# Kernel optimization log

Measured on AMD Instinct MI355X. Metric: run time of the kernel, lower is better.

## Reference

```python
import jax, jax.numpy as jnp
import numpy as np

MC = 16384
N_STEPS = 120
PERIOD = 30
N_MAT = 4
N_STR = 21
WIDTH_DIFF = 50
WIDTH_VAN = 30
WIDTH_EXO = 20
N_HIDDEN = 3  # n_layers=4 -> input layer + 3 hidden layers + output layer
R = 0.05
TIMEGRID = jnp.asarray(np.linspace(0.0, 1.0, N_STEPS + 1).astype(np.float32))
STRIKES = jnp.asarray(np.linspace(0.8, 1.2, N_STR).astype(np.float32))


def _init_net(key, d_in, width, d_out):
    ks = jax.random.split(key, 6)
    f = lambda k, shape, fan: jax.random.normal(k, shape, jnp.float32) / np.sqrt(fan).astype(np.float32)
    return dict(
        W0=f(ks[0], (N_MAT, d_in, width), d_in),
        b0=f(ks[1], (N_MAT, width), width),
        hW=f(ks[2], (N_MAT, N_HIDDEN, width, width), width),
        hb=f(ks[3], (N_MAT, N_HIDDEN, width), width),
        Wo=f(ks[4], (N_MAT, width, d_out), width),
        bo=f(ks[5], (N_MAT, d_out), width),
    )


def setup_inputs() -> dict:
    key = jax.random.key(0)
    kz, kd, kv, ke = jax.random.split(key, 4)
    inp = {
        "S0": jnp.ones((1,), jnp.float32),
        "z": jax.random.normal(kz, (MC, N_STEPS), jnp.float32),
    }
    for name, net in (("d", _init_net(kd, 2, WIDTH_DIFF, 1)),
                      ("v", _init_net(kv, 2, WIDTH_VAN, N_STR * N_MAT)),
                      ("e", _init_net(ke, N_STEPS + 2, WIDTH_EXO, 1))):
        for pn, arr in net.items():
            inp[name + pn] = arr
    inp["MC_samples"] = MC
    inp["ind_T"] = N_STEPS
    inp["period_length"] = PERIOD
    return inp


def _mlp(x, W0, b0, hW, hb, Wo, bo, softplus_out):
    h = jax.nn.relu(x @ W0 + b0)
    for k in range(hW.shape[0]):  # static small number of hidden layers
        h = jax.nn.relu(h @ hW[k] + hb[k])
    y = h @ Wo + bo
    return jax.nn.softplus(y) if softplus_out else y


def _forward(S0, z, dW0, db0, dhW, dhb, dWo, dbo,
             vW0, vb0, vhW, vhb, vWo, vbo,
             eW0, eb0, ehW, ehb, eWo, ebo,
             MC_samples, ind_T, period_length, remat=False):
    sg = jax.lax.stop_gradient
    S_init = jnp.ones((MC_samples, 1), jnp.float32) * S0
    path0 = jnp.zeros((MC_samples, N_STEPS + 1), jnp.float32).at[:, 0].set(S_init[:, 0])
    zeros_mat = jnp.zeros((N_MAT, N_STR), jnp.float32)

    def step(carry, i):
        S_old, cv_v, cv_e, run_max, path, pv, pvv = carry
        idx = (i - 1) // period_length
        t0 = TIMEGRID[i - 1]
        h = TIMEGRID[i] - TIMEGRID[i - 1]
        sqh = jnp.sqrt(h)
        dWn = sqh * jax.lax.dynamic_slice_in_dim(z, i - 1, 1, 1)  # (MC,1)
        t = jnp.full_like(S_old, t0)
        diff = _mlp(jnp.concatenate([t, S_old], 1),
                    dW0[idx], db0[idx], dhW[idx], dhb[idx], dWo[idx], dbo[idx], True)
        Sd, diffd = sg(S_old), sg(diff)
        S_new = (S_old
                 + R * S_old * h / (1.0 + R * Sd * sqh)
                 + S_old * diff * dWn / (1.0 + Sd * diffd * sqh))
        disc = jnp.exp(-R * t0)
        cv_v = cv_v + disc * Sd * diffd * dWn * _mlp(
            jnp.concatenate([t, Sd], 1),
            vW0[idx], vb0[idx], vhW[idx], vhb[idx], vWo[idx], vbo[idx], False)
        cv_e = cv_e + disc * Sd * diffd * dWn * _mlp(
            jnp.concatenate([t, path], 1),
            eW0[idx], eb0[idx], ehW[idx], ehb[idx], eWo[idx], ebo[idx], False)
        path = jax.lax.dynamic_update_slice(path, sg(S_new), (0, i))
        run_max = jnp.maximum(run_max, S_new)
        # vanilla prices at maturities (i multiple of period_length)
        ind_m = i // period_length - 1
        disc_i = jnp.exp(-R * TIMEGRID[i])
        cv_row = jax.lax.dynamic_slice_in_dim(
            cv_v.reshape(MC_samples, N_MAT, N_STR), ind_m, 1, 1)[:, 0, :]
        pr = disc_i * jnp.maximum(S_new - STRIKES[None, :], 0.0) - cv_row  # (MC, N_STR)
        is_mat = (i % period_length) == 0
        pv = jnp.where(is_mat, jax.lax.dynamic_update_index_in_dim(pv, pr.mean(0), ind_m, 0), pv)
        pvv = jnp.where(is_mat, jax.lax.dynamic_update_index_in_dim(pvv, jnp.var(pr, axis=0, ddof=1), ind_m, 0), pvv)
        return (S_new, cv_v, cv_e, run_max, path, pv, pvv), None

    body = jax.checkpoint(step) if remat else step
    carry0 = (S_init,
              jnp.zeros((MC_samples, N_STR * N_MAT), jnp.float32),
              jnp.zeros((MC_samples, 1), jnp.float32),
              S_init, path0, zeros_mat, zeros_mat)
    (S_T, cv_v, cv_e, run_max, path, pv, pvv), _ = jax.lax.scan(
        body, carry0, jnp.arange(1, ind_T + 1))

    sgv = jax.lax.stop_gradient
    exotic = run_max - S_T
    discT = jnp.exp(-R * TIMEGRID[ind_T])
    e = discT * exotic
    error = sgv(e) - jnp.mean(sgv(e)) - sgv(cv_e)
    price_exo = e - cv_e
    return pv, pvv, price_exo, price_exo.mean(), jnp.var(price_exo, ddof=1), error


def reference(S0, z, dW0, db0, dhW, dhb, dWo, dbo,
              vW0, vb0, vhW, vhb, vWo, vbo,
              eW0, eb0, ehW, ehb, eWo, ebo,
              MC_samples, ind_T, period_length):
    return _forward(S0, z, dW0, db0, dhW, dhb, dWo, dbo,
                    vW0, vb0, vhW, vhb, vWo, vbo,
                    eW0, eb0, ehW, ehb, eWo, ebo,
                    MC_samples, ind_T, period_length)
```

## Files before the change

kernel.cpp:

```cpp
#include <hip/hip_runtime.h>
#include <math.h>

#define MC      16384
#define NSTEPS  120
#define PER     30
#define NMAT    4
#define NSTR    21
#define RRATE   0.05f
#define NBLK    512
#define NSAMP   32

typedef short short8  __attribute__((ext_vector_type(8)));
typedef short short4v __attribute__((ext_vector_type(4)));
typedef float f32x4   __attribute__((ext_vector_type(4)));

#define WS_PRPART 0
#define WS_EPART  (NMAT*NSTR*2*NBLK)
#define WS_MEANE  (WS_EPART + NBLK)

#define OUT_PV    0
#define OUT_PVV   84
#define OUT_PEXO  168
#define OUT_MEAN  16552
#define OUT_VAR   16553
#define OUT_ERR   16554

__device__ __forceinline__ float tgridf(int i)  { return (float)((double)i * (1.0/120.0)); }
__device__ __forceinline__ float strikef(int s) { return (float)(0.8 + (double)s * 0.02); }
__device__ __forceinline__ float softplusf(float x){
  return fmaxf(x, 0.0f) + log1pf(expf(-fabsf(x)));
}
__device__ __forceinline__ unsigned short f2bf(float f){
  unsigned u = __builtin_bit_cast(unsigned, f);
  unsigned r = (u + 0x7FFFu + ((u>>16)&1u)) >> 16;
  return (unsigned short)r;
}
__device__ __forceinline__ float bf2f(unsigned short u){
  return __builtin_bit_cast(float, ((unsigned)u)<<16);
}
__device__ __forceinline__ int swaddr(int row, int slot, int inner){
  return row*256 + (((slot + row) & 15) << 4) + inner;
}
__device__ __forceinline__ short8 rdA(const unsigned short* H, int mt, int base, int lane){
  int addr = swaddr(mt*16 + (lane&15), base + (lane>>4), 0);
  return *(const short8*)((const char*)H + addr);
}
__device__ __forceinline__ f32x4 mm(short8 a, short8 b, f32x4 c){
  return __builtin_amdgcn_mfma_f32_16x16x32_bf16(a, b, c, 0, 0, 0);
}
__device__ __forceinline__ void stD(unsigned short* H, int colbase, int mt, int lane,
                                    f32x4 acc, float bias, bool relu){
  int col  = colbase + (lane & 15);
  int slot = col >> 3, inner = (col & 7)*2;
  #pragma unroll
  for (int i2=0;i2<4;++i2){
    int rw = mt*16 + ((lane>>4)<<2) + i2;
    float v = acc[i2] + bias;
    if (relu) v = fmaxf(v, 0.0f);
    *(unsigned short*)((char*)H + swaddr(rw, slot, inner)) = f2bf(v);
  }
}
__device__ __forceinline__ short8 mkB(const float* __restrict__ W, int ldn, int KV, int NV,
                                      int kt, int n0, int lane){
  short8 r;
  #pragma unroll
  for (int i2=0;i2<8;++i2){
    int k = kt*32 + ((lane>>4)<<3) + i2;
    int n = n0 + (lane & 15);
    float w = (k<KV && n<NV) ? W[k*ldn + n] : 0.0f;
    r[i2] = (short)f2bf(w);
  }
  return r;
}

extern "C" __global__ void __launch_bounds__(256,2) mc_main(
    const float* __restrict__ S0p, const float* __restrict__ z,
    const float* __restrict__ dW0, const float* __restrict__ db0,
    const float* __restrict__ dhW, const float* __restrict__ dhb,
    const float* __restrict__ dWo, const float* __restrict__ dbo,
    const float* __restrict__ vW0, const float* __restrict__ vb0,
    const float* __restrict__ vhW, const float* __restrict__ vhb,
    const float* __restrict__ vWo, const float* __restrict__ vbo,
    const float* __restrict__ eW0, const float* __restrict__ eb0,
    const float* __restrict__ ehW, const float* __restrict__ ehb,
    const float* __restrict__ eWo, const float* __restrict__ ebo,
    float* __restrict__ out, float* __restrict__ ws)
{
  __shared__ unsigned short Hb0[NSAMP*128];
  __shared__ unsigned short Hb1[NSAMP*128];
  __shared__ float vh3f[NSAMP*40];
  __shared__ float zper[NSAMP*30];
  __shared__ float eW0per[NMAT*600];
  __shared__ float dW0s[NMAT*128];
  __shared__ float db0s[NMAT*64];
  __shared__ float vW0s[NMAT*64];
  __shared__ float vb0s[NMAT*32];
  __shared__ float eW0ts[NMAT*20];
  __shared__ float eb0s[NMAT*20];
  __shared__ float dWoL[64];
  __shared__ float eWoL[32];
  __shared__ float Sb[NSAMP], Cb[NSAMP], ebuf[NSAMP];
  __shared__ float part[2*84*2];

  const int tid  = threadIdx.x;
  const int lane = tid & 63;
  const int wid  = __builtin_amdgcn_readfirstlane(tid >> 6);
  const int blk  = blockIdx.x;
  const int r    = tid >> 3;
  const int cc   = tid & 7;

  for (int q=tid; q<NMAT*128; q+=256){ int mat=q>>7, rw=(q>>6)&1, j=q&63; dW0s[q] = (j<50)? dW0[mat*100+rw*50+j] : 0.f; }
  for (int q=tid; q<NMAT*64;  q+=256){ int mat=q>>6, j=q&63;              db0s[q] = (j<50)? db0[mat*50+j] : 0.f; }
  for (int q=tid; q<NMAT*64;  q+=256){ int mat=q>>6, rw=(q>>5)&1, j=q&31; vW0s[q] = (j<30)? vW0[mat*60+rw*30+j] : 0.f; }
  for (int q=tid; q<NMAT*32;  q+=256){ int mat=q>>5, j=q&31;              vb0s[q] = (j<30)? vb0[mat*30+j] : 0.f; }
  if (tid < NMAT*20){ int mat=tid/20, j=tid%20; eW0ts[tid]=eW0[mat*2440+j]; eb0s[tid]=eb0[mat*20+j]; }

  const int  ntd = wid;
  const bool isv = (wid < 2);
  const int  ntq = wid & 1;

  const float S0v = S0p[0];
  float S = S0v, runmax = S0v, cvE = 0.f, C = 0.f;
  f32x4 rr[3];
  #pragma unroll
  for (int q=0;q<3;++q){ rr[q][0]=0.f; rr[q][1]=0.f; rr[q][2]=0.f; rr[q][3]=0.f; }
  float aE[NMAT][4];
  #pragma unroll
  for (int mt2=0;mt2<NMAT;++mt2){ aE[mt2][0]=0.f; aE[mt2][1]=0.f; aE[mt2][2]=0.f; aE[mt2][3]=0.f; }
  float G_[4] = {0.f,0.f,0.f,0.f};

  #pragma unroll 1
  for (int p=0;p<NMAT;++p){
    for (int q=tid; q<NSAMP*30; q+=256){ int r2=q/30, c2=q%30; zper[q] = z[(size_t)(blk*NSAMP+r2)*NSTEPS + p*30 + c2]; }
    for (int q=tid; q<NMAT*600; q+=256){ int mat=q/600, k=q%600; eW0per[q] = eW0[mat*2440 + p*600 + 20 + k]; }
    if (tid < 64)              dWoL[tid] = (tid<50)? dWo[p*50+tid] : 0.f;
    else if (tid < 96){ int j=tid-64; eWoL[j] = (j<20)? eWo[p*20+j] : 0.f; }

    const float dboS = dbo[p], eboS = ebo[p];

    const float* dhWp = dhW + p*7500;
    short8 Bd00 = mkB(dhWp,      50,50,50, 0, ntd*16, lane);
    short8 Bd01 = mkB(dhWp,      50,50,50, 1, ntd*16, lane);
    short8 Bd10 = mkB(dhWp+2500, 50,50,50, 0, ntd*16, lane);
    short8 Bd11 = mkB(dhWp+2500, 50,50,50, 1, ntd*16, lane);
    short8 Bd20 = mkB(dhWp+5000, 50,50,50, 0, ntd*16, lane);
    short8 Bd21 = mkB(dhWp+5000, 50,50,50, 1, ntd*16, lane);
    const int nd = ntd*16 + (lane&15);
    float biasD0 = (nd<50)? dhb[p*150 +      nd] : 0.f;
    float biasD1 = (nd<50)? dhb[p*150 + 50 + nd] : 0.f;
    float biasD2 = (nd<50)? dhb[p*150 +100 + nd] : 0.f;
    const float* qW    = isv ? (vhW + p*2700) : (ehW + p*1200);
    const int    qstep = isv ? 900 : 400;
    const int    qN    = isv ? 30  : 20;
    short8 Bq0 = mkB(qW,         qN,qN,qN, 0, ntq*16, lane);
    short8 Bq1 = mkB(qW+qstep,   qN,qN,qN, 0, ntq*16, lane);
    short8 Bq2 = mkB(qW+2*qstep, qN,qN,qN, 0, ntq*16, lane);
    const float* qb = isv ? (vhb + p*90) : (ehb + p*60);
    const int nq = ntq*16 + (lane&15);
    float biasQ0 = (nq<qN)? qb[       nq] : 0.f;
    float biasQ1 = (nq<qN)? qb[qN   + nq] : 0.f;
    float biasQ2 = (nq<qN)? qb[2*qN + nq] : 0.f;

    const int qbase = isv ? 8 : 12;
    const int qcolb = (isv?64:96) + ntq*16;

    __syncthreads();

    #pragma unroll 1
    for (int ii=1; ii<=PER; ++ii){
      const float t0  = tgridf(p*PER + ii - 1);
      const float t1  = tgridf(p*PER + ii);
      const float h   = t1 - t0;
      const float sqh = sqrtf(h);

      {
        short8 hv;
        #pragma unroll
        for (int k=0;k<8;++k){
          int j = cc*8 + k;
          float u = fmaxf(fmaf(t0, dW0s[p*128+j], fmaf(S, dW0s[p*128+64+j], db0s[p*64+j])), 0.f);
          hv[k] = (short)f2bf(u);
        }
        *(short8*)((char*)Hb0 + swaddr(r, cc, 0)) = hv;
        short4v vv;
        #pragma unroll
        for (int k=0;k<4;++k){
          int j = cc*4 + k;
          float u = fmaxf(fmaf(t0, vW0s[p*64+j], fmaf(S, vW0s[p*64+32+j], vb0s[p*32+j])), 0.f);
          vv[k] = (short)f2bf(u);
        }
        *(short4v*)((char*)Hb0 + swaddr(r, 8+(cc>>1), (cc&1)*8)) = vv;
        short4v ev = {0,0,0,0};
        if (cc < 5){
          const int o = (ii-1)*20 + cc*4;
          f32x4 w0 = *(const f32x4*)&eW0per[        o];
          f32x4 w1 = *(const f32x4*)&eW0per[ 600 +  o];
          f32x4 w2 = *(const f32x4*)&eW0per[1200 +  o];
          f32x4 w3 = *(const f32x4*)&eW0per[1800 +  o];
          #pragma unroll
          for (int k=0;k<4;++k){
            aE[0][k] = fmaf(S, w0[k], aE[0][k]);
            aE[1][k] = fmaf(S, w1[k], aE[1][k]);
            aE[2][k] = fmaf(S, w2[k], aE[2][k]);
            aE[3][k] = fmaf(S, w3[k], aE[3][k]);
            float a = (p==0)?aE[0][k]:(p==1)?aE[1][k]:(p==2)?aE[2][k]:aE[3][k];
            int j = cc*4 + k;
            float e0 = fmaxf(t0*eW0ts[p*20+j] + a + eb0s[p*20+j], 0.f);
            ev[k] = (short)f2bf(e0);
          }
        }
        *(short4v*)((char*)Hb0 + swaddr(r, 12+(cc>>1), (cc&1)*8)) = ev;
      }
      __syncthreads();
      {
        short8 a00=rdA(Hb0,0,0,lane), a01=rdA(Hb0,0,4,lane);
        short8 a10=rdA(Hb0,1,0,lane), a11=rdA(Hb0,1,4,lane);
        f32x4 c0={0.f,0.f,0.f,0.f}, c1={0.f,0.f,0.f,0.f};
        c0=mm(a00,Bd00,c0); c0=mm(a01,Bd01,c0);
        c1=mm(a10,Bd00,c1); c1=mm(a11,Bd01,c1);
        stD(Hb1, ntd*16, 0, lane, c0, biasD0, true);
        stD(Hb1, ntd*16, 1, lane, c1, biasD0, true);
        short8 q0=rdA(Hb0,0,qbase,lane), q1=rdA(Hb0,1,qbase,lane);
        f32x4 cq0={0.f,0.f,0.f,0.f}, cq1={0.f,0.f,0.f,0.f};
        cq0=mm(q0,Bq0,cq0); cq1=mm(q1,Bq0,cq1);
        stD(Hb1, qcolb, 0, lane, cq0, biasQ0, true);
        stD(Hb1, qcolb, 1, lane, cq1, biasQ0, true);
      }
      __syncthreads();
      {
        short8 a00=rdA(Hb1,0,0,lane), a01=rdA(Hb1,0,4,lane);
        short8 a10=rdA(Hb1,1,0,lane), a11=rdA(Hb1,1,4,lane);
        f32x4 c0={0.f,0.f,0.f,0.f}, c1={0.f,0.f,0.f,0.f};
        c0=mm(a00,Bd10,c0); c0=mm(a01,Bd11,c0);
        c1=mm(a10,Bd10,c1); c1=mm(a11,Bd11,c1);
        stD(Hb0, ntd*16, 0, lane, c0, biasD1, true);
        stD(Hb0, ntd*16, 1, lane, c1, biasD1, true);
        short8 q0=rdA(Hb1,0,qbase,lane), q1=rdA(Hb1,1,qbase,lane);
        f32x4 cq0={0.f,0.f,0.f,0.f}, cq1={0.f,0.f,0.f,0.f};
        cq0=mm(q0,Bq1,cq0); cq1=mm(q1,Bq1,cq1);
        stD(Hb0, qcolb, 0, lane, cq0, biasQ1, true);
        stD(Hb0, qcolb, 1, lane, cq1, biasQ1, true);
      }
      __syncthreads();
      {
        short8 a00=rdA(Hb0,0,0,lane), a01=rdA(Hb0,0,4,lane);
        short8 a10=rdA(Hb0,1,0,lane), a11=rdA(Hb0,1,4,lane);
        f32x4 c0={0.f,0.f,0.f,0.f}, c1={0.f,0.f,0.f,0.f};
        c0=mm(a00,Bd20,c0); c0=mm(a01,Bd21,c0);
        c1=mm(a10,Bd20,c1); c1=mm(a11,Bd21,c1);
        stD(Hb1, ntd*16, 0, lane, c0, biasD2, true);
        stD(Hb1, ntd*16, 1, lane, c1, biasD2, true);
        short8 q0=rdA(Hb0,0,qbase,lane), q1=rdA(Hb0,1,qbase,lane);
        f32x4 cq0={0.f,0.f,0.f,0.f}, cq1={0.f,0.f,0.f,0.f};
        cq0=mm(q0,Bq2,cq0); cq1=mm(q1,Bq2,cq1);
        if (isv){
          #pragma unroll
          for (int i2=0;i2<4;++i2){
            int r0 = ((lane>>4)<<2) + i2;
            vh3f[ r0      *40 + ntq*16 + (lane&15)] = fmaxf(cq0[i2] + biasQ2, 0.f);
            vh3f[(16+r0)  *40 + ntq*16 + (lane&15)] = fmaxf(cq1[i2] + biasQ2, 0.f);
          }
        } else {
          stD(Hb1, qcolb, 0, lane, cq0, biasQ2, true);
          stD(Hb1, qcolb, 1, lane, cq1, biasQ2, true);
        }
      }
      __syncthreads();
      {
        float yp = 0.f;
        {
          short8 hv = *(const short8*)((const char*)Hb1 + swaddr(r, cc, 0));
          #pragma unroll
          for (int k=0;k<8;++k) yp = fmaf(bf2f((unsigned short)hv[k]), dWoL[cc*8+k], yp);
        }
        float yep = 0.f;
        if (cc < 5){
          short4v hv = *(const short4v*)((const char*)Hb1 + swaddr(r, 12+(cc>>1), (cc&1)*8));
          #pragma unroll
          for (int k=0;k<4;++k) yep = fmaf(bf2f((unsigned short)hv[k]), eWoL[cc*4+k], yep);
        }
        #pragma unroll
        for (int mk=1; mk<8; mk<<=1){ yp += __shfl_xor(yp, mk); yep += __shfl_xor(yep, mk); }
        const float y    = yp + dboS;
        const float diff = softplusf(y);
        const float zv   = zper[r*30 + (ii-1)];
        const float dWn  = sqh * zv;
        const float d1 = 1.f + RRATE*S*sqh;
        const float d2 = 1.f + S*diff*sqh;
        const float Snew = S + RRATE*S*h/d1 + S*diff*dWn/d2;
        const float disc = expf(-RRATE*t0);
        const float coef = disc * S * diff * dWn;
        cvE = fmaf(coef, yep + eboS, cvE);
        C += coef;
        runmax = fmaxf(runmax, Snew);
        {
          f32x4 vv = *(const f32x4*)&vh3f[r*40 + cc*4];
          #pragma unroll
          for (int k=0;k<4;++k) G_[k] = fmaf(coef, vv[k], G_[k]);
        }
        S = Snew;

        if (ii==PER){
          short4v gv;
          #pragma unroll
          for (int k=0;k<4;++k){ gv[k] = (short)f2bf(G_[k]); G_[k] = 0.f; }
          *(short4v*)((char*)Hb0 + swaddr(r, cc>>1, (cc&1)*8)) = gv;
          if (cc==0){ Sb[r] = S; Cb[r] = C; }
          C = 0.f;
        }
      }

      if (ii==PER){
        __syncthreads();
        const float disc_i = expf(-RRATE*t1);
        const float* vWop = vWo + p*2520;
        const float* vbop = vbo + p*84;
        #pragma unroll
        for (int q3=0;q3<3;++q3){
          const int T = wid*3 + q3;
          const int mtr = T/6, ntr = T%6;
          short8 a = rdA(Hb0, mtr, 0, lane);
          const int col = ntr*16 + (lane&15);
          short8 bw;
          #pragma unroll
          for (int i2=0;i2<8;++i2){
            int k = ((lane>>4)<<3)+i2;
            float w = (k<30 && col<84) ? vWop[k*84+col] : 0.f;
            bw[i2] = (short)f2bf(w);
          }
          f32x4 d4 = {0.f,0.f,0.f,0.f};
          d4 = mm(a,bw,d4);
          const float vb = (col<84)? vbop[col] : 0.f;
          const int s = col - p*NSTR;
          const bool inr = (s>=0) && (s<NSTR) && (col<84);
          const float K = strikef(s);
          float ssum=0.f, ssq=0.f;
          #pragma unroll
          for (int i2=0;i2<4;++i2){
            int row = mtr*16 + ((lane>>4)<<2) + i2;
            rr[q3][i2] += d4[i2] + Cb[row]*vb;
            if (inr){
              float pr = disc_i*fmaxf(Sb[row]-K,0.f) - rr[q3][i2];
              ssum += pr; ssq = fmaf(pr,pr,ssq);
            }
          }
          ssum += __shfl_down(ssum,16); ssum += __shfl_down(ssum,32);
          ssq  += __shfl_down(ssq ,16); ssq  += __shfl_down(ssq ,32);
          if (inr && lane<16){
            part[(mtr*84+col)*2+0] = ssum;
            part[(mtr*84+col)*2+1] = ssq;
          }
        }
        __syncthreads();
        if (tid < NSTR){
          int cidx = p*NSTR + tid;
          ws[WS_PRPART + (cidx*2+0)*NBLK + blk] = part[cidx*2] + part[(84+cidx)*2];
        } else if (tid >= 64 && tid < 64+NSTR){
          int cidx = p*NSTR + (tid-64);
          ws[WS_PRPART + (cidx*2+1)*NBLK + blk] = part[cidx*2+1] + part[(84+cidx)*2+1];
        }
      }
    }
  }

  if (cc==0){
    const float discT = expf(-RRATE);
    const float e = discT * (runmax - S);
    out[OUT_PEXO + blk*NSAMP + r] = e - cvE;
    ebuf[r] = e;
  }
  __syncthreads();
  if (tid < 32){
    float se = ebuf[tid];
    se += __shfl_down(se,16); se += __shfl_down(se,8);
    se += __shfl_down(se,4);  se += __shfl_down(se,2); se += __shfl_down(se,1);
    if (tid==0) ws[WS_EPART + blk] = se;
  }
}

extern "C" __global__ void fin_pv(const float* __restrict__ ws, float* __restrict__ out){
  const int t = threadIdx.x;
  if (t >= NMAT*NSTR) return;
  float sum=0.0f, ssq=0.0f;
  for (int b=0;b<NBLK;++b){
    sum += ws[WS_PRPART + (t*2+0)*NBLK + b];
    ssq += ws[WS_PRPART + (t*2+1)*NBLK + b];
  }
  out[OUT_PV  + t] = sum * (1.0f/MC);
  out[OUT_PVV + t] = (ssq - sum*sum*(1.0f/MC)) * (1.0f/(MC-1));
}

extern "C" __global__ void fin_pe(float* out, float* ws){
  __shared__ float sA[4], sB[4], sC[4];
  const int t = threadIdx.x;
  float sum=0.0f, ssq=0.0f;
  for (int idx=t; idx<MC; idx+=256){
    const float v = out[OUT_PEXO+idx];
    sum += v; ssq = fmaf(v,v,ssq);
  }
  float es = ws[WS_EPART + t] + ws[WS_EPART + 256 + t];
  for (int o=32;o>0;o>>=1){
    sum += __shfl_down(sum,o);
    ssq += __shfl_down(ssq,o);
    es  += __shfl_down(es,o);
  }
  const int w=t>>6, lane=t&63;
  if (lane==0){ sA[w]=sum; sB[w]=ssq; sC[w]=es; }
  __syncthreads();
  if (t==0){
    const float s=sA[0]+sA[1]+sA[2]+sA[3];
    const float q=sB[0]+sB[1]+sB[2]+sB[3];
    const float e=sC[0]+sC[1]+sC[2]+sC[3];
    out[OUT_MEAN]=s*(1.0f/MC);
    out[OUT_VAR]=(q - s*s*(1.0f/MC))*(1.0f/(MC-1));
    ws[WS_MEANE]=e*(1.0f/MC);
  }
}

extern "C" __global__ void fin_err(float* out, const float* __restrict__ ws){
  const int m = blockIdx.x*blockDim.x + threadIdx.x;
  if (m < MC) out[OUT_ERR+m] = out[OUT_PEXO+m] - ws[WS_MEANE];
}

extern "C" void kernel_launch(void* const* d_in, const int* in_sizes, int n_in,
                              void* d_out, int out_size, void* d_ws, size_t ws_size,
                              hipStream_t stream){
  (void)in_sizes; (void)n_in; (void)out_size; (void)ws_size;
  const float* S0 =(const float*)d_in[0];
  const float* z  =(const float*)d_in[1];
  const float* dW0=(const float*)d_in[2];
  const float* db0=(const float*)d_in[3];
  const float* dhW=(const float*)d_in[4];
  const float* dhb=(const float*)d_in[5];
  const float* dWo=(const float*)d_in[6];
  const float* dbo=(const float*)d_in[7];
  const float* vW0=(const float*)d_in[8];
  const float* vb0=(const float*)d_in[9];
  const float* vhW=(const float*)d_in[10];
  const float* vhb=(const float*)d_in[11];
  const float* vWo=(const float*)d_in[12];
  const float* vbo=(const float*)d_in[13];
  const float* eW0=(const float*)d_in[14];
  const float* eb0=(const float*)d_in[15];
  const float* ehW=(const float*)d_in[16];
  const float* ehb=(const float*)d_in[17];
  const float* eWo=(const float*)d_in[18];
  const float* ebo=(const float*)d_in[19];
  float* out=(float*)d_out;
  float* ws =(float*)d_ws;

  mc_main<<<dim3(NBLK),dim3(256),0,stream>>>(S0,z,dW0,db0,dhW,dhb,dWo,dbo,
                                             vW0,vb0,vhW,vhb,vWo,vbo,
                                             eW0,eb0,ehW,ehb,eWo,ebo,out,ws);
  fin_pv <<<dim3(1), dim3(128),0,stream>>>(ws,out);
  fin_pe <<<dim3(1), dim3(256),0,stream>>>(out,ws);
  fin_err<<<dim3(64),dim3(256),0,stream>>>(out,ws);
}
```

Before: 489.4 us.

## Fold MLP biases into MFMA via constant-one column and spill B-fragments to LDS

Adds a constant 1 feature column to each hidden activation tile and places each layer's bias in the matching weight row, so the MFMA computes the bias. This removes per-element bias adds and the separate C accumulator and Cb buffer for the van output. Some B fragments (third diffusion layer and the Q-net weights) now live in LDS instead of registers, which lowers VGPR pressure but adds LDS reads in every step. The approach depends on bf16 rounding of the bias, which changes numerics slightly, and on spare padded columns being free.

```diff
diff --git a/kernel.cpp b/kernel.cpp
--- a/kernel.cpp
+++ b/kernel.cpp
@@ -49,25 +49,43 @@
   return __builtin_amdgcn_mfma_f32_16x16x32_bf16(a, b, c, 0, 0, 0);
 }
 __device__ __forceinline__ void stD(unsigned short* H, int colbase, int mt, int lane,
-                                    f32x4 acc, float bias, bool relu){
+                                    f32x4 acc, bool relu){
   int col  = colbase + (lane & 15);
   int slot = col >> 3, inner = (col & 7)*2;
   #pragma unroll
   for (int i2=0;i2<4;++i2){
     int rw = mt*16 + ((lane>>4)<<2) + i2;
-    float v = acc[i2] + bias;
+    float v = acc[i2];
     if (relu) v = fmaxf(v, 0.0f);
     *(unsigned short*)((char*)H + swaddr(rw, slot, inner)) = f2bf(v);
   }
 }
-__device__ __forceinline__ short8 mkB(const float* __restrict__ W, int ldn, int KV, int NV,
-                                      int kt, int n0, int lane){
+__device__ __forceinline__ short8 mkBd(const float* __restrict__ W, const float* __restrict__ bias,
+                                       int n0, int kt, int lane){
   short8 r;
+  int n = n0 + (lane&15);
   #pragma unroll
   for (int i2=0;i2<8;++i2){
     int k = kt*32 + ((lane>>4)<<3) + i2;
-    int n = n0 + (lane & 15);
-    float w = (k<KV && n<NV) ? W[k*ldn + n] : 0.0f;
+    float w;
+    if (k<50)       w = (n<50)? W[k*50+n] : 0.f;
+    else if (k==50) w = (n<50)? bias[n] : ((n==50)? 1.f : 0.f);
+    else            w = 0.f;
+    r[i2] = (short)f2bf(w);
+  }
+  return r;
+}
+__device__ __forceinline__ short8 mkBq(const float* __restrict__ W, const float* __restrict__ bias,
+                                       int KV, int n0, int lane){
+  short8 r;
+  int n = n0 + (lane&15);
+  #pragma unroll
+  for (int i2=0;i2<8;++i2){
+    int k = ((lane>>4)<<3) + i2;
+    float w;
+    if (k<KV)       w = (n<KV)? W[k*KV+n] : 0.f;
+    else if (k==KV) w = (n<KV)? bias[n] : ((n==KV)? 1.f : 0.f);
+    else            w = 0.f;
     r[i2] = (short)f2bf(w);
   }
   return r;
@@ -88,6 +106,8 @@
 {
   __shared__ unsigned short Hb0[NSAMP*128];
   __shared__ unsigned short Hb1[NSAMP*128];
+  __shared__ short8 BqL[4][3][64];
+  __shared__ short8 BdL[4][2][64];
   __shared__ float vh3f[NSAMP*40];
   __shared__ float zper[NSAMP*30];
   __shared__ float eW0per[NMAT*600];
@@ -99,7 +119,7 @@
   __shared__ float eb0s[NMAT*20];
   __shared__ float dWoL[64];
   __shared__ float eWoL[32];
-  __shared__ float Sb[NSAMP], Cb[NSAMP], ebuf[NSAMP];
+  __shared__ float Sb[NSAMP], ebuf[NSAMP];
   __shared__ float part[2*84*2];
 
   const int tid  = threadIdx.x;
@@ -110,9 +130,9 @@
   const int cc   = tid & 7;
 
   for (int q=tid; q<NMAT*128; q+=256){ int mat=q>>7, rw=(q>>6)&1, j=q&63; dW0s[q] = (j<50)? dW0[mat*100+rw*50+j] : 0.f; }
-  for (int q=tid; q<NMAT*64;  q+=256){ int mat=q>>6, j=q&63;              db0s[q] = (j<50)? db0[mat*50+j] : 0.f; }
+  for (int q=tid; q<NMAT*64;  q+=256){ int mat=q>>6, j=q&63;              db0s[q] = (j<50)? db0[mat*50+j] : ((j==50)? 1.f : 0.f); }
   for (int q=tid; q<NMAT*64;  q+=256){ int mat=q>>6, rw=(q>>5)&1, j=q&31; vW0s[q] = (j<30)? vW0[mat*60+rw*30+j] : 0.f; }
-  for (int q=tid; q<NMAT*32;  q+=256){ int mat=q>>5, j=q&31;              vb0s[q] = (j<30)? vb0[mat*30+j] : 0.f; }
+  for (int q=tid; q<NMAT*32;  q+=256){ int mat=q>>5, j=q&31;              vb0s[q] = (j<30)? vb0[mat*30+j] : ((j==30)? 1.f : 0.f); }
   if (tid < NMAT*20){ int mat=tid/20, j=tid%20; eW0ts[tid]=eW0[mat*2440+j]; eb0s[tid]=eb0[mat*20+j]; }
 
   const int  ntd = wid;
@@ -120,7 +140,7 @@
   const int  ntq = wid & 1;
 
   const float S0v = S0p[0];
-  float S = S0v, runmax = S0v, cvE = 0.f, C = 0.f;
+  float S = S0v, runmax = S0v, cvE = 0.f;
   f32x4 rr[3];
   #pragma unroll
   for (int q=0;q<3;++q){ rr[q][0]=0.f; rr[q][1]=0.f; rr[q][2]=0.f; rr[q][3]=0.f; }
@@ -139,28 +159,22 @@
     const float dboS = dbo[p], eboS = ebo[p];
 
     const float* dhWp = dhW + p*7500;
-    short8 Bd00 = mkB(dhWp,      50,50,50, 0, ntd*16, lane);
-    short8 Bd01 = mkB(dhWp,      50,50,50, 1, ntd*16, lane);
-    short8 Bd10 = mkB(dhWp+2500, 50,50,50, 0, ntd*16, lane);
-    short8 Bd11 = mkB(dhWp+2500, 50,50,50, 1, ntd*16, lane);
-    short8 Bd20 = mkB(dhWp+5000, 50,50,50, 0, ntd*16, lane);
-    short8 Bd21 = mkB(dhWp+5000, 50,50,50, 1, ntd*16, lane);
-    const int nd = ntd*16 + (lane&15);
-    float biasD0 = (nd<50)? dhb[p*150 +      nd] : 0.f;
-    float biasD1 = (nd<50)? dhb[p*150 + 50 + nd] : 0.f;
-    float biasD2 = (nd<50)? dhb[p*150 +100 + nd] : 0.f;
-    const float* qW    = isv ? (vhW + p*2700) : (ehW + p*1200);
-    const int    qstep = isv ? 900 : 400;
-    const int    qN    = isv ? 30  : 20;
-    short8 Bq0 = mkB(qW,         qN,qN,qN, 0, ntq*16, lane);
-    short8 Bq1 = mkB(qW+qstep,   qN,qN,qN, 0, ntq*16, lane);
-    short8 Bq2 = mkB(qW+2*qstep, qN,qN,qN, 0, ntq*16, lane);
-    const float* qb = isv ? (vhb + p*90) : (ehb + p*60);
-    const int nq = ntq*16 + (lane&15);
-    float biasQ0 = (nq<qN)? qb[       nq] : 0.f;
-    float biasQ1 = (nq<qN)? qb[qN   + nq] : 0.f;
-    float biasQ2 = (nq<qN)? qb[2*qN + nq] : 0.f;
-
+    const float* dhbp = dhb + p*150;
+    short8 Bd00 = mkBd(dhWp,      dhbp,     ntd*16, 0, lane);
+    short8 Bd01 = mkBd(dhWp,      dhbp,     ntd*16, 1, lane);
+    short8 Bd10 = mkBd(dhWp+2500, dhbp+50,  ntd*16, 0, lane);
+    short8 Bd11 = mkBd(dhWp+2500, dhbp+50,  ntd*16, 1, lane);
+    BdL[wid][0][lane] = mkBd(dhWp+5000, dhbp+100, ntd*16, 0, lane);
+    BdL[wid][1][lane] = mkBd(dhWp+5000, dhbp+100, ntd*16, 1, lane);
+    {
+      const float* qW    = isv ? (vhW + p*2700) : (ehW + p*1200);
+      const float* qb    = isv ? (vhb + p*90)   : (ehb + p*60);
+      const int    qstep = isv ? 900 : 400;
+      const int    qN    = isv ? 30  : 20;
+      BqL[wid][0][lane] = mkBq(qW,         qb,        qN, ntq*16, lane);
+      BqL[wid][1][lane] = mkBq(qW+qstep,   qb+qN,     qN, ntq*16, lane);
+      BqL[wid][2][lane] = mkBq(qW+2*qstep, qb+2*qN,   qN, ntq*16, lane);
+    }
     const int qbase = isv ? 8 : 12;
     const int qcolb = (isv?64:96) + ntq*16;
 
@@ -208,6 +222,8 @@
             float e0 = fmaxf(t0*eW0ts[p*20+j] + a + eb0s[p*20+j], 0.f);
             ev[k] = (short)f2bf(e0);
           }
+        } else if (cc == 5){
+          ev[0] = (short)0x3F80;
         }
         *(short4v*)((char*)Hb0 + swaddr(r, 12+(cc>>1), (cc&1)*8)) = ev;
       }
@@ -218,13 +234,14 @@
         f32x4 c0={0.f,0.f,0.f,0.f}, c1={0.f,0.f,0.f,0.f};
         c0=mm(a00,Bd00,c0); c0=mm(a01,Bd01,c0);
         c1=mm(a10,Bd00,c1); c1=mm(a11,Bd01,c1);
-        stD(Hb1, ntd*16, 0, lane, c0, biasD0, true);
-        stD(Hb1, ntd*16, 1, lane, c1, biasD0, true);
+        stD(Hb1, ntd*16, 0, lane, c0, true);
+        stD(Hb1, ntd*16, 1, lane, c1, true);
+        short8 Bq = BqL[wid][0][lane];
         short8 q0=rdA(Hb0,0,qbase,lane), q1=rdA(Hb0,1,qbase,lane);
         f32x4 cq0={0.f,0.f,0.f,0.f}, cq1={0.f,0.f,0.f,0.f};
-        cq0=mm(q0,Bq0,cq0); cq1=mm(q1,Bq0,cq1);
-        stD(Hb1, qcolb, 0, lane, cq0, biasQ0, true);
-        stD(Hb1, qcolb, 1, lane, cq1, biasQ0, true);
+        cq0=mm(q0,Bq,cq0); cq1=mm(q1,Bq,cq1);
+        stD(Hb1, qcolb, 0, lane, cq0, true);
+        stD(Hb1, qcolb, 1, lane, cq1, true);
       }
       __syncthreads();
       {
@@ -233,36 +250,39 @@
         f32x4 c0={0.f,0.f,0.f,0.f}, c1={0.f,0.f,0.f,0.f};
         c0=mm(a00,Bd10,c0); c0=mm(a01,Bd11,c0);
         c1=mm(a10,Bd10,c1); c1=mm(a11,Bd11,c1);
-        stD(Hb0, ntd*16, 0, lane, c0, biasD1, true);
-        stD(Hb0, ntd*16, 1, lane, c1, biasD1, true);
+        stD(Hb0, ntd*16, 0, lane, c0, true);
+        stD(Hb0, ntd*16, 1, lane, c1, true);
+        short8 Bq = BqL[wid][1][lane];
         short8 q0=rdA(Hb1,0,qbase,lane), q1=rdA(Hb1,1,qbase,lane);
         f32x4 cq0={0.f,0.f,0.f,0.f}, cq1={0.f,0.f,0.f,0.f};
-        cq0=mm(q0,Bq1,cq0); cq1=mm(q1,Bq1,cq1);
-        stD(Hb0, qcolb, 0, lane, cq0, biasQ1, true);
-        stD(Hb0, qcolb, 1, lane, cq1, biasQ1, true);
+        cq0=mm(q0,Bq,cq0); cq1=mm(q1,Bq,cq1);
+        stD(Hb0, qcolb, 0, lane, cq0, true);
+        stD(Hb0, qcolb, 1, lane, cq1, true);
       }
       __syncthreads();
       {
+        short8 b20 = BdL[wid][0][lane], b21 = BdL[wid][1][lane];
         short8 a00=rdA(Hb0,0,0,lane), a01=rdA(Hb0,0,4,lane);
         short8 a10=rdA(Hb0,1,0,lane), a11=rdA(Hb0,1,4,lane);
         f32x4 c0={0.f,0.f,0.f,0.f}, c1={0.f,0.f,0.f,0.f};
-        c0=mm(a00,Bd20,c0); c0=mm(a01,Bd21,c0);
-        c1=mm(a10,Bd20,c1); c1=mm(a11,Bd21,c1);
-        stD(Hb1, ntd*16, 0, lane, c0, biasD2, true);
-        stD(Hb1, ntd*16, 1, lane, c1, biasD2, true);
+        c0=mm(a00,b20,c0); c0=mm(a01,b21,c0);
+        c1=mm(a10,b20,c1); c1=mm(a11,b21,c1);
+        stD(Hb1, ntd*16, 0, lane, c0, true);
+        stD(Hb1, ntd*16, 1, lane, c1, true);
+        short8 Bq = BqL[wid][2][lane];
         short8 q0=rdA(Hb0,0,qbase,lane), q1=rdA(Hb0,1,qbase,lane);
         f32x4 cq0={0.f,0.f,0.f,0.f}, cq1={0.f,0.f,0.f,0.f};
-        cq0=mm(q0,Bq2,cq0); cq1=mm(q1,Bq2,cq1);
+        cq0=mm(q0,Bq,cq0); cq1=mm(q1,Bq,cq1);
         if (isv){
           #pragma unroll
           for (int i2=0;i2<4;++i2){
             int r0 = ((lane>>4)<<2) + i2;
-            vh3f[ r0      *40 + ntq*16 + (lane&15)] = fmaxf(cq0[i2] + biasQ2, 0.f);
-            vh3f[(16+r0)  *40 + ntq*16 + (lane&15)] = fmaxf(cq1[i2] + biasQ2, 0.f);
+            vh3f[ r0     *40 + ntq*16 + (lane&15)] = fmaxf(cq0[i2], 0.f);
+            vh3f[(16+r0) *40 + ntq*16 + (lane&15)] = fmaxf(cq1[i2], 0.f);
           }
         } else {
-          stD(Hb1, qcolb, 0, lane, cq0, biasQ2, true);
-          stD(Hb1, qcolb, 1, lane, cq1, biasQ2, true);
+          stD(Hb1, qcolb, 0, lane, cq0, true);
+          stD(Hb1, qcolb, 1, lane, cq1, true);
         }
       }
       __syncthreads();
@@ -291,7 +311,6 @@
         const float disc = expf(-RRATE*t0);
         const float coef = disc * S * diff * dWn;
         cvE = fmaf(coef, yep + eboS, cvE);
-        C += coef;
         runmax = fmaxf(runmax, Snew);
         {
           f32x4 vv = *(const f32x4*)&vh3f[r*40 + cc*4];
@@ -305,8 +324,7 @@
           #pragma unroll
           for (int k=0;k<4;++k){ gv[k] = (short)f2bf(G_[k]); G_[k] = 0.f; }
           *(short4v*)((char*)Hb0 + swaddr(r, cc>>1, (cc&1)*8)) = gv;
-          if (cc==0){ Sb[r] = S; Cb[r] = C; }
-          C = 0.f;
+          if (cc==0) Sb[r] = S;
         }
       }
 
@@ -325,12 +343,15 @@
           #pragma unroll
           for (int i2=0;i2<8;++i2){
             int k = ((lane>>4)<<3)+i2;
-            float w = (k<30 && col<84) ? vWop[k*84+col] : 0.f;
+            float w = 0.f;
+            if (col < 84){
+              if (k < 30)       w = vWop[k*84+col];
+              else if (k == 30) w = vbop[col];
+            }
             bw[i2] = (short)f2bf(w);
           }
           f32x4 d4 = {0.f,0.f,0.f,0.f};
           d4 = mm(a,bw,d4);
-          const float vb = (col<84)? vbop[col] : 0.f;
           const int s = col - p*NSTR;
           const bool inr = (s>=0) && (s<NSTR) && (col<84);
           const float K = strikef(s);
@@ -338,7 +359,7 @@
           #pragma unroll
           for (int i2=0;i2<4;++i2){
             int row = mtr*16 + ((lane>>4)<<2) + i2;
-            rr[q3][i2] += d4[i2] + Cb[row]*vb;
+            rr[q3][i2] += d4[i2];
             if (inr){
               float pr = disc_i*fmaxf(Sb[row]-K,0.f) - rr[q3][i2];
               ssum += pr; ssq = fmaf(pr,pr,ssq);
```

Result: faster. 469.2 us (-4.1%).
